# Kernel tuning notes

Measured on AMD Instinct MI355X. Metric: run time of the kernel, lower is better.

Reference implementation:

```python
import jax, jax.numpy as jnp
import numpy as np

H = 16  # num_heads (inner_dim 1024 // default head_dim 64)
D = 64  # head_dim
EPS = 1e-5

def layernorm(x, w, b):
    mu = jnp.mean(x, axis=-1, keepdims=True)
    var = jnp.var(x, axis=-1, keepdims=True)
    return (x - mu) * jax.lax.rsqrt(var + EPS) * w + b

def attention(x, kv, wq, wk, wv, wo, bo):
    b, t, c = x.shape
    s = kv.shape[1]
    q = (x @ wq).reshape(b, t, H, D).transpose(0, 2, 1, 3)   # bhtd
    k = (kv @ wk).reshape(b, s, H, D).transpose(0, 2, 1, 3)  # bhsd
    v = (kv @ wv).reshape(b, s, H, D).transpose(0, 2, 1, 3)
    scores = jnp.einsum('bhqd,bhkd->bhqk', q, k) * (D ** -0.5)
    attn = jax.nn.softmax(scores, axis=-1)
    out = jnp.einsum('bhqk,bhkd->bhqd', attn, v)
    out = out.transpose(0, 2, 1, 3).reshape(b, t, c)
    return out @ wo + bo

def setup_inputs() -> dict:
    key = jax.random.key(0)
    ks = jax.random.split(key, 16)
    hs = 1024
    dff = 4 * hs  # 4096
    sc = lambda fan_in: 1.0 / np.sqrt(fan_in)
    inp = {
        'x': jax.random.normal(ks[0], (2, 2048, hs), jnp.float32),
        'encoder_hidden_states': jax.random.normal(ks[1], (2, 512, 64), jnp.float32),
        'ln1_w': jnp.ones((hs,), jnp.float32), 'ln1_b': jnp.zeros((hs,), jnp.float32),
        'a1_wq': jax.random.normal(ks[2], (hs, hs), jnp.float32) * sc(hs),
        'a1_wk': jax.random.normal(ks[3], (hs, hs), jnp.float32) * sc(hs),
        'a1_wv': jax.random.normal(ks[4], (hs, hs), jnp.float32) * sc(hs),
        'a1_wo': jax.random.normal(ks[5], (hs, hs), jnp.float32) * sc(hs),
        'a1_bo': jnp.zeros((hs,), jnp.float32),
        'ln2_w': jnp.ones((hs,), jnp.float32), 'ln2_b': jnp.zeros((hs,), jnp.float32),
        'a2_wq': jax.random.normal(ks[6], (hs, hs), jnp.float32) * sc(hs),
        'a2_wk': jax.random.normal(ks[7], (64, hs), jnp.float32) * sc(64),
        'a2_wv': jax.random.normal(ks[8], (64, hs), jnp.float32) * sc(64),
        'a2_wo': jax.random.normal(ks[9], (hs, hs), jnp.float32) * sc(hs),
        'a2_bo': jnp.zeros((hs,), jnp.float32),
        'ln3_w': jnp.ones((hs,), jnp.float32), 'ln3_b': jnp.zeros((hs,), jnp.float32),
        'ff_w1': jax.random.normal(ks[10], (hs, 2 * dff), jnp.float32) * sc(hs),
        'ff_b1': jnp.zeros((2 * dff,), jnp.float32),
        'ff_w2': jax.random.normal(ks[11], (dff, hs), jnp.float32) * sc(dff),
        'ff_b2': jnp.zeros((hs,), jnp.float32),
    }
    return inp

def reference(x, encoder_hidden_states, ln1_w, ln1_b, a1_wq, a1_wk, a1_wv, a1_wo, a1_bo,
              ln2_w, ln2_b, a2_wq, a2_wk, a2_wv, a2_wo, a2_bo,
              ln3_w, ln3_b, ff_w1, ff_b1, ff_w2, ff_b2):
    # self-attention sub-block
    h = layernorm(x, ln1_w, ln1_b)
    x = x + attention(h, h, a1_wq, a1_wk, a1_wv, a1_wo, a1_bo)
    # cross-attention sub-block (kv from encoder_hidden_states, dim 64)
    h = layernorm(x, ln2_w, ln2_b)
    x = x + attention(h, encoder_hidden_states, a2_wq, a2_wk, a2_wv, a2_wo, a2_bo)
    # GEGLU feed-forward sub-block
    h = layernorm(x, ln3_w, ln3_b)
    hp = h @ ff_w1 + ff_b1
    h1, h2 = jnp.split(hp, 2, axis=-1)
    h = (h1 * jax.nn.gelu(h2, approximate=False)) @ ff_w2 + ff_b2
    return x + h
```

## Files before the change

kernel.cpp:

```cpp
#include <hip/hip_runtime.h>
#include <hip/hip_bf16.h>
#include <stdint.h>

typedef unsigned short u16;
typedef __bf16 bf16x8 __attribute__((ext_vector_type(8)));
typedef float f32x4 __attribute__((ext_vector_type(4)));
typedef u16 u16x8 __attribute__((ext_vector_type(8)));
typedef u16 u16x4 __attribute__((ext_vector_type(4)));

__device__ __forceinline__ u16 f2bf(float f) {
  union { float f; uint32_t u; } v; v.f = f;
  uint32_t r = v.u + 0x7fffu + ((v.u >> 16) & 1u);
  return (u16)(r >> 16);
}
__device__ __forceinline__ float bf2f(u16 u) {
  union { uint32_t u; float f; } v; v.u = ((uint32_t)u) << 16;
  return v.f;
}
__device__ __forceinline__ uint32_t cvtpk(float a, float b) {
  uint32_t r;
  asm("v_cvt_pk_bf16_f32 %0, %1, %2" : "=v"(r) : "v"(a), "v"(b));
  return r;
}

__device__ __forceinline__ void gld16(const u16* g, u16* l) {
  __builtin_amdgcn_global_load_lds(
      (const __attribute__((address_space(1))) uint32_t*)g,
      (__attribute__((address_space(3))) uint32_t*)l, 16, 0, 0);
}

struct WB {
  const float* src[6];
  u16* dst[6];
  float scale[6];
};
__global__ void wconv_b(WB wb, int K, int N) {
  const int z = blockIdx.z;
  const float* __restrict__ W = wb.src[z];
  u16* __restrict__ Wt = wb.dst[z];
  const float scale = wb.scale[z];
  __shared__ float tile[32][33];
  const int n0 = blockIdx.x * 32, k0 = blockIdx.y * 32;
  const int tx = threadIdx.x, ty = threadIdx.y;
#pragma unroll
  for (int i = 0; i < 4; ++i)
    tile[ty + 8 * i][tx] = W[(size_t)(k0 + ty + 8 * i) * N + n0 + tx];
  __syncthreads();
#pragma unroll
  for (int i = 0; i < 4; ++i)
    Wt[(size_t)(n0 + ty + 8 * i) * K + k0 + tx] = f2bf(scale * tile[tx][ty + 8 * i]);
}

__global__ void wconv_t(const float* __restrict__ W, u16* __restrict__ Wt, int K, int N) {
  __shared__ float tile[32][33];
  const int n0 = blockIdx.x * 32, k0 = blockIdx.y * 32;
  const int tx = threadIdx.x, ty = threadIdx.y;
#pragma unroll
  for (int i = 0; i < 4; ++i)
    tile[ty + 8 * i][tx] = W[(size_t)(k0 + ty + 8 * i) * N + n0 + tx];
  __syncthreads();
#pragma unroll
  for (int i = 0; i < 4; ++i)
    Wt[(size_t)(n0 + ty + 8 * i) * K + k0 + tx] = f2bf(tile[tx][ty + 8 * i]);
}

__global__ void wconv_g(const float* __restrict__ W, u16* __restrict__ Wt) {
  __shared__ float tile[32][33];
  const int n0 = blockIdx.x * 32, k0 = blockIdx.y * 32;
  const int tx = threadIdx.x, ty = threadIdx.y;
#pragma unroll
  for (int i = 0; i < 4; ++i)
    tile[ty + 8 * i][tx] = W[(size_t)(k0 + ty + 8 * i) * 8192 + n0 + tx];
  __syncthreads();
#pragma unroll
  for (int i = 0; i < 4; ++i) {
    const int n = n0 + ty + 8 * i;
    const int half = n >> 12, c = n & 4095;
    const int blk = c >> 7, cc = c & 127;
    const int wcol = cc >> 5, rem = cc & 31;
    const int sub = rem >> 4, idx = rem & 15;
    const int p = blk * 256 + wcol * 64 + (sub * 2 + half) * 16 + idx;
    Wt[(size_t)p * 1024 + k0 + tx] = f2bf(tile[tx][ty + 8 * i]);
  }
}

__global__ void cvt_bf(const float* __restrict__ in, u16* __restrict__ out, int n) {
  int i = blockIdx.x * 256 + threadIdx.x;
  if (i < n) out[i] = f2bf(in[i]);
}

__global__ __launch_bounds__(256)
void vtrans(const u16* __restrict__ V, int ldv, int hoff, u16* __restrict__ Vt, int S) {
  __shared__ u16 tile[64][72];
  const int t0 = blockIdx.x, bh = blockIdx.y;
  const int b = bh >> 4, hc = (bh & 15) * 64 + hoff;
  const int tid = threadIdx.x;
  const int r = tid >> 2, dq = (tid & 3) * 16;
  const int pos = ((r >> 5) << 5) | (((r >> 2) & 3) << 3) | (((r >> 4) & 1) << 2) | (r & 3);
  const size_t grow = ((size_t)b * S + t0 * 64 + r) * ldv + hc + dq;
  u16x8 v1 = *(const u16x8*)&V[grow];
  u16x8 v2 = *(const u16x8*)&V[grow + 8];
#pragma unroll
  for (int j = 0; j < 8; ++j) {
    tile[dq + j][pos] = v1[j];
    tile[dq + 8 + j][pos] = v2[j];
  }
  __syncthreads();
  const int d = tid >> 2, c = (tid & 3) * 16;
  u16x8 o1, o2;
#pragma unroll
  for (int j = 0; j < 8; ++j) { o1[j] = tile[d][c + j]; o2[j] = tile[d][c + 8 + j]; }
  *(u16x8*)&Vt[((size_t)bh * 64 + d) * S + t0 * 64 + c] = o1;
  *(u16x8*)&Vt[((size_t)bh * 64 + d) * S + t0 * 64 + c + 8] = o2;
}

__global__ __launch_bounds__(256)
void ln_fwd(const float* __restrict__ X, const float* __restrict__ wt,
            const float* __restrict__ bs, u16* __restrict__ Y) {
  const int row = blockIdx.x, t = threadIdx.x;
  const float4 v = *(const float4*)&X[(size_t)row * 1024 + t * 4];
  float s = v.x + v.y + v.z + v.w;
  float s2 = v.x * v.x + v.y * v.y + v.z * v.z + v.w * v.w;
#pragma unroll
  for (int off = 32; off > 0; off >>= 1) {
    s += __shfl_xor(s, off);
    s2 += __shfl_xor(s2, off);
  }
  __shared__ float rs[4], rs2[4];
  const int w = t >> 6;
  if ((t & 63) == 0) { rs[w] = s; rs2[w] = s2; }
  __syncthreads();
  s = rs[0] + rs[1] + rs[2] + rs[3];
  s2 = rs2[0] + rs2[1] + rs2[2] + rs2[3];
  const float mu = s * (1.0f / 1024.0f);
  const float var = s2 * (1.0f / 1024.0f) - mu * mu;
  const float rstd = rsqrtf(var + 1e-5f);
  const float4 wv = *(const float4*)&wt[t * 4];
  const float4 bv = *(const float4*)&bs[t * 4];
  u16x4 o;
  o[0] = f2bf((v.x - mu) * rstd * wv.x + bv.x);
  o[1] = f2bf((v.y - mu) * rstd * wv.y + bv.y);
  o[2] = f2bf((v.z - mu) * rstd * wv.z + bv.z);
  o[3] = f2bf((v.w - mu) * rstd * wv.w + bv.w);
  *(u16x4*)&Y[(size_t)row * 1024 + t * 4] = o;
}

#define GSTAGE(kt, bufi)                                                         \
  {                                                                              \
    _Pragma("unroll")                                                            \
    for (int p = 0; p < 4; ++p) {                                                \
      int idx = p * 256 + tid;                                                   \
      int row = idx >> 3, c = idx & 7;                                           \
      gld16(A + (size_t)(bm + row) * lda + (kt) * 64 + ((c ^ (row & 7)) << 3),   \
            &Al[bufi][idx * 8]);                                                 \
    }                                                                            \
    _Pragma("unroll")                                                            \
    for (int p = 0; p < TN / 32; ++p) {                                          \
      int idx = p * 256 + tid;                                                   \
      int row = idx >> 3, c = idx & 7;                                           \
      gld16(Bt + (size_t)(bn + row) * K + (kt) * 64 + ((c ^ (row & 7)) << 3),    \
            &Bl[bufi][idx * 8]);                                                 \
    }                                                                            \
  }

template<int TN>
__global__ __launch_bounds__(256, 3)
void gemm_bf16(const u16* __restrict__ A, int lda, const u16* __restrict__ Bt,
               int M, int N, int K, const float* __restrict__ bias,
               const float* __restrict__ resid, float oscale,
               float* __restrict__ outF, u16* __restrict__ outB) {
  constexpr int WNV = (TN == 128) ? 2 : 1;
  constexpr int WMV = 4 / WNV;
  constexpr int WM = 128 / WMV;
  constexpr int WN = TN / WNV;
  constexpr int MI = WM / 16, NI = WN / 16;
  __shared__ __align__(16) u16 Al[2][128 * 64];
  __shared__ __align__(16) u16 Bl[2][TN * 64];
  const int tid = threadIdx.x;
  const int w = tid >> 6, l = tid & 63, lo = l & 15, g = l >> 4;
  const int gx = gridDim.x, nwg = gx * gridDim.y;
  const int lin = blockIdx.y * gx + blockIdx.x;
  const int q = nwg >> 3, r = nwg & 7;
  const int xcd = lin & 7, pos = lin >> 3;
  const int sid = (xcd < r ? xcd * (q + 1) : r * (q + 1) + (xcd - r) * q) + pos;
  const int bm = (sid % gx) * 128, bn = (sid / gx) * TN;
  const int wm = (w / WNV) * WM, wn = (w % WNV) * WN;
  const int swz = (lo & 7) << 3;
  const int NT = K >> 6;
  f32x4 acc[MI][NI] = {};

  GSTAGE(0, 0);
  asm volatile("s_waitcnt vmcnt(0)" ::: "memory");
  __syncthreads();

  for (int t = 0; t < NT; ++t) {
    const int cur = t & 1;
    if (t + 1 < NT) GSTAGE(t + 1, cur ^ 1);
#pragma unroll
    for (int ks = 0; ks < 2; ++ks) {
      bf16x8 af[MI], bf[NI];
#pragma unroll
      for (int i = 0; i < MI; ++i)
        af[i] = *(const bf16x8*)&Al[cur][(wm + i * 16 + lo) * 64 + ((ks * 32 + g * 8) ^ swz)];
#pragma unroll
      for (int i = 0; i < NI; ++i)
        bf[i] = *(const bf16x8*)&Bl[cur][(wn + i * 16 + lo) * 64 + ((ks * 32 + g * 8) ^ swz)];
#pragma unroll
      for (int mi = 0; mi < MI; ++mi)
#pragma unroll
        for (int ni = 0; ni < NI; ++ni)
          acc[mi][ni] = __builtin_amdgcn_mfma_f32_16x16x32_bf16(af[mi], bf[ni], acc[mi][ni], 0, 0, 0);
    }
    asm volatile("s_waitcnt vmcnt(0)" ::: "memory");
    __syncthreads();
  }

#pragma unroll
  for (int mi = 0; mi < MI; ++mi) {
#pragma unroll
    for (int ni = 0; ni < NI; ++ni) {
      const int col = bn + wn + ni * 16 + lo;
      const float bb = bias ? bias[col] : 0.0f;
      const int row0 = bm + wm + mi * 16 + g * 4;
#pragma unroll
      for (int rr = 0; rr < 4; ++rr) {
        const size_t off = (size_t)(row0 + rr) * N + col;
        float v = acc[mi][ni][rr] * oscale + bb;
        if (resid) v += resid[off];
        if (outF) outF[off] = v;
        else outB[off] = f2bf(v);
      }
    }
  }
}

#define ST2(p0, p1, dst) { gld16(p0, (dst) + tid * 8); gld16(p1, (dst) + 4096 + tid * 8); (p0) += 64; (p1) += 64; }

template<int MODE>
__global__ __launch_bounds__(512, 2)
void gemm256(const u16* __restrict__ A, int lda, const u16* __restrict__ Bt,
             int M, int N, int K, const float* __restrict__ bias,
             const float* __restrict__ resid, float oscale,
             float* __restrict__ outF, u16* __restrict__ outB) {
  __shared__ __align__(16) u16 sm[65536];
  const int tid = threadIdx.x;
  const int w = tid >> 6, l = tid & 63, lo = l & 15, g = l >> 4;
  const int wrow = w >> 2, wcol = w & 3;
  const int gx = gridDim.x;
  const int nwg = gx * gridDim.y;
  const int lin = blockIdx.y * gx + blockIdx.x;
  const int q = nwg >> 3, r = nwg & 7;
  const int xcd = lin & 7, pos = lin >> 3;
  const int sid = (xcd < r ? xcd * (q + 1) : r * (q + 1) + (xcd - r) * q) + pos;
  const int bm = (sid % gx) * 256, bn = (sid / gx) * 256;

  const int NT = K >> 6;
  const int swz = (lo & 7) << 3;
  f32x4 acc[8][4] = {};

  const int sr8 = tid >> 3;
  const int sc8 = ((tid & 7) ^ (sr8 & 7)) << 3;
  const u16 *pA0 = A + (size_t)(bm + sr8) * lda + sc8;
  const u16 *pA1 = A + (size_t)(bm + 64 + sr8) * lda + sc8;
  const u16 *pA2 = A + (size_t)(bm + 128 + sr8) * lda + sc8;
  const u16 *pA3 = A + (size_t)(bm + 192 + sr8) * lda + sc8;
  const u16 *pB0 = Bt + (size_t)(bn + sr8) * K + sc8;
  const u16 *pB1 = Bt + (size_t)(bn + 64 + sr8) * K + sc8;
  const u16 *pB2 = Bt + (size_t)(bn + 128 + sr8) * K + sc8;
  const u16 *pB3 = Bt + (size_t)(bn + 192 + sr8) * K + sc8;

  ST2(pB0, pB1, sm + 16384);
  ST2(pB2, pB3, sm + 16384 + 8192);
  ST2(pA0, pA1, sm);
  ST2(pA2, pA3, sm + 8192);
  if (NT > 1) {
    ST2(pB0, pB1, sm + 32768 + 16384);
    ST2(pB2, pB3, sm + 32768 + 16384 + 8192);
    ST2(pA0, pA1, sm + 32768);
  }
  asm volatile("s_waitcnt vmcnt(6)" ::: "memory");
  __builtin_amdgcn_s_barrier();

  for (int t = 0; t < NT; ++t) {
    u16* Ab_ = sm + (t & 1) * 32768;
    u16* Bb_ = Ab_ + 16384;
    bf16x8 a0[4][2], a1[4][2], bfr[4][2];
#pragma unroll
    for (int mf = 0; mf < 4; ++mf) {
      const int rowi = wrow * 128 + mf * 16 + lo;
#pragma unroll
      for (int kk = 0; kk < 2; ++kk)
        a0[mf][kk] = *(const bf16x8*)&Ab_[rowi * 64 + ((kk * 32 + g * 8) ^ swz)];
    }
#pragma unroll
    for (int nf = 0; nf < 4; ++nf) {
      const int rowi = wcol * 64 + nf * 16 + lo;
#pragma unroll
      for (int kk = 0; kk < 2; ++kk)
        bfr[nf][kk] = *(const bf16x8*)&Bb_[rowi * 64 + ((kk * 32 + g * 8) ^ swz)];
    }
    if (t + 1 < NT)
      ST2(pA2, pA3, sm + ((t + 1) & 1) * 32768 + 8192);
    __builtin_amdgcn_s_barrier();
    __builtin_amdgcn_s_setprio(1);
#pragma unroll
    for (int mf = 0; mf < 4; ++mf)
#pragma unroll
      for (int nf = 0; nf < 2; ++nf)
#pragma unroll
        for (int kk = 0; kk < 2; ++kk)
          acc[mf][nf] = __builtin_amdgcn_mfma_f32_16x16x32_bf16(a0[mf][kk], bfr[nf][kk], acc[mf][nf], 0, 0, 0);
    __builtin_amdgcn_s_setprio(0);
    __builtin_amdgcn_s_barrier();
#pragma unroll
    for (int mf = 0; mf < 4; ++mf) {
      const int rowi = wrow * 128 + 64 + mf * 16 + lo;
#pragma unroll
      for (int kk = 0; kk < 2; ++kk)
        a1[mf][kk] = *(const bf16x8*)&Ab_[rowi * 64 + ((kk * 32 + g * 8) ^ swz)];
    }
    if (t + 2 < NT)
      ST2(pB0, pB1, sm + (t & 1) * 32768 + 16384);
    __builtin_amdgcn_s_barrier();
    __builtin_amdgcn_s_setprio(1);
#pragma unroll
    for (int mf = 0; mf < 4; ++mf)
#pragma unroll
      for (int nf = 2; nf < 4; ++nf)
#pragma unroll
        for (int kk = 0; kk < 2; ++kk)
          acc[mf][nf] = __builtin_amdgcn_mfma_f32_16x16x32_bf16(a0[mf][kk], bfr[nf][kk], acc[mf][nf], 0, 0, 0);
    __builtin_amdgcn_s_setprio(0);
    __builtin_amdgcn_s_barrier();
    if (t + 2 < NT)
      ST2(pB2, pB3, sm + (t & 1) * 32768 + 16384 + 8192);
    __builtin_amdgcn_s_barrier();
    __builtin_amdgcn_s_setprio(1);
#pragma unroll
    for (int mf = 0; mf < 4; ++mf)
#pragma unroll
      for (int nf = 0; nf < 2; ++nf)
#pragma unroll
        for (int kk = 0; kk < 2; ++kk)
          acc[4 + mf][nf] = __builtin_amdgcn_mfma_f32_16x16x32_bf16(a1[mf][kk], bfr[nf][kk], acc[4 + mf][nf], 0, 0, 0);
    __builtin_amdgcn_s_setprio(0);
    __builtin_amdgcn_s_barrier();
    if (t + 2 < NT)
      ST2(pA0, pA1, sm + (t & 1) * 32768);
    __builtin_amdgcn_s_barrier();
    __builtin_amdgcn_s_setprio(1);
#pragma unroll
    for (int mf = 0; mf < 4; ++mf)
#pragma unroll
      for (int nf = 2; nf < 4; ++nf)
#pragma unroll
        for (int kk = 0; kk < 2; ++kk)
          acc[4 + mf][nf] = __builtin_amdgcn_mfma_f32_16x16x32_bf16(a1[mf][kk], bfr[nf][kk], acc[4 + mf][nf], 0, 0, 0);
    __builtin_amdgcn_s_setprio(0);
    if (t + 2 < NT) asm volatile("s_waitcnt vmcnt(6)" ::: "memory");
    else            asm volatile("s_waitcnt vmcnt(0)" ::: "memory");
    __builtin_amdgcn_s_barrier();
  }

  if (MODE == 1) {
    const int obase = bn >> 1;
#pragma unroll
    for (int mi = 0; mi < 8; ++mi) {
#pragma unroll
      for (int sub = 0; sub < 2; ++sub) {
        const int col = obase + wcol * 32 + sub * 16 + lo;
        const float b1 = bias[col];
        const float b2 = bias[4096 + col];
#pragma unroll
        for (int rr = 0; rr < 4; ++rr) {
          const int rowi = wrow * 128 + mi * 16 + g * 4 + rr;
          const float h1 = acc[mi][sub * 2][rr] + b1;
          const float h2 = acc[mi][sub * 2 + 1][rr] + b2;
          const float ge = 0.5f * h2 * (1.0f + erff(h2 * 0.70710678118f));
          outB[(size_t)(bm + rowi) * 4096 + col] = f2bf(h1 * ge);
        }
      }
    }
    return;
  }

#pragma unroll
  for (int mi = 0; mi < 8; ++mi) {
#pragma unroll
    for (int ni = 0; ni < 4; ++ni) {
      const int col = bn + wcol * 64 + ni * 16 + lo;
      const float bb = bias ? bias[col] : 0.0f;
      const int row0 = bm + wrow * 128 + mi * 16 + g * 4;
#pragma unroll
      for (int rr = 0; rr < 4; ++rr) {
        const size_t off = (size_t)(row0 + rr) * N + col;
        float v = acc[mi][ni][rr] * oscale + bb;
        if (resid) v += resid[off];
        if (outF) outF[off] = v;
        else outB[off] = f2bf(v);
      }
    }
  }
}

#define ABODY(TT, KST, KRD, VST, VRD, SCur, SNxt)                                  \
  {                                                                                \
    if ((TT) + 2 < ntile) {                                                        \
      gld16(kp0, &KST[tid * 8]);                                                   \
      gld16(kp1, &KST[2048 + tid * 8]);                                            \
      kp0 += kadv; kp1 += kadv;                                                    \
    }                                                                              \
    if ((TT) + 1 < ntile) {                                                        \
      gld16(vp0, &VST[tid * 8]);                                                   \
      gld16(vp1, &VST[2048 + tid * 8]);                                            \
      vp0 += 64; vp1 += 64;                                                        \
    }                                                                              \
    if ((TT) + 2 < ntile)      asm volatile("s_waitcnt vmcnt(4)" ::: "memory");    \
    else if ((TT) + 1 < ntile) asm volatile("s_waitcnt vmcnt(2)" ::: "memory");    \
    else                       asm volatile("s_waitcnt vmcnt(0)" ::: "memory");    \
    __builtin_amdgcn_s_barrier();                                                  \
    if ((TT) + 1 < ntile) {                                                        \
      _Pragma("unroll")                                                            \
      for (int c = 0; c < 4; ++c) {                                                \
        f32x4 zz = {};                                                             \
        SNxt[c] = zz;                                                              \
        _Pragma("unroll")                                                          \
        for (int kk = 0; kk < 2; ++kk) {                                           \
          bf16x8 kf = *(const bf16x8*)&KRD[(c * 16 + lo) * 64 +                    \
                                           ((kk * 32 + g * 8) ^ ((lo & 7) << 3))]; \
          SNxt[c] = __builtin_amdgcn_mfma_f32_16x16x32_bf16(kf, qf[kk], SNxt[c], 0, 0, 0); \
        }                                                                          \
      }                                                                            \
    }                                                                              \
    float mx = fmaxf(fmaxf(fmaxf(SCur[0][0], SCur[0][1]), fmaxf(SCur[0][2], SCur[0][3])),  \
                     fmaxf(fmaxf(SCur[1][0], SCur[1][1]), fmaxf(SCur[1][2], SCur[1][3]))); \
    mx = fmaxf(mx, fmaxf(fmaxf(fmaxf(SCur[2][0], SCur[2][1]), fmaxf(SCur[2][2], SCur[2][3])),  \
                         fmaxf(fmaxf(SCur[3][0], SCur[3][1]), fmaxf(SCur[3][2], SCur[3][3])))); \
    mx = fmaxf(mx, __shfl_xor(mx, 16));                                            \
    mx = fmaxf(mx, __shfl_xor(mx, 32));                                            \
    if (!__all(mx <= m + 8.0f)) {                                                  \
      const float mn = fmaxf(m, mx);                                               \
      const float al = exp2f(m - mn);                                              \
      m = mn;                                                                      \
      f32x4 arv;                                                                   \
      _Pragma("unroll")                                                            \
      for (int rr = 0; rr < 4; ++rr) arv[rr] = __shfl(al, 20 * g + rr);            \
      _Pragma("unroll")                                                            \
      for (int dn = 0; dn < 4; ++dn) oa[dn] *= arv;                                \
      lrow *= arv;                                                                 \
    }                                                                              \
    _Pragma("unroll")                                                              \
    for (int c = 0; c < 4; ++c)                                                    \
      _Pragma("unroll")                                                            \
      for (int rr = 0; rr < 4; ++rr)                                               \
        SCur[c][rr] = exp2f(SCur[c][rr] - m);                                      \
    union { uint32_t u[4]; bf16x8 v; } af[2];                                      \
    _Pragma("unroll")                                                              \
    for (int ks = 0; ks < 2; ++ks) {                                               \
      af[ks].u[0] = cvtpk(SCur[2 * ks][0], SCur[2 * ks][1]);                       \
      af[ks].u[1] = cvtpk(SCur[2 * ks][2], SCur[2 * ks][3]);                       \
      af[ks].u[2] = cvtpk(SCur[2 * ks + 1][0], SCur[2 * ks + 1][1]);               \
      af[ks].u[3] = cvtpk(SCur[2 * ks + 1][2], SCur[2 * ks + 1][3]);               \
    }                                                                              \
    lrow = __builtin_amdgcn_mfma_f32_16x16x32_bf16(af[0].v, onesc.v, lrow, 0, 0, 0); \
    lrow = __builtin_amdgcn_mfma_f32_16x16x32_bf16(af[1].v, onesc.v, lrow, 0, 0, 0); \
    _Pragma("unroll")                                                              \
    for (int dn = 0; dn < 4; ++dn)                                                 \
      _Pragma("unroll")                                                            \
      for (int ks = 0; ks < 2; ++ks) {                                             \
        bf16x8 vf = *(const bf16x8*)&VRD[(dn * 16 + lo) * 64 +                     \
                                         ((ks * 32 + g * 8) ^ ((lo & 7) << 3))];   \
        oa[dn] = __builtin_amdgcn_mfma_f32_16x16x32_bf16(af[ks].v, vf, oa[dn], 0, 0, 0); \
      }                                                                            \
    asm volatile("s_waitcnt lgkmcnt(0)" ::: "memory");                             \
    __builtin_amdgcn_s_barrier();                                                  \
  }

__global__ __launch_bounds__(256, 4)
void attn_fwd(const u16* __restrict__ Q, int ldq, const u16* __restrict__ K, int ldk,
              const u16* __restrict__ Vt, u16* __restrict__ O, int T, int S) {
  __shared__ __align__(16) u16 Kl[2][4096];
  __shared__ __align__(16) u16 Vl[2][4096];
  const int tid = threadIdx.x, w = tid >> 6, l = tid & 63, lo = l & 15, g = l >> 4;
  const int nwg = gridDim.x * gridDim.y;
  const int n = blockIdx.y * gridDim.x + blockIdx.x;
  const int sid = (n & 7) * (nwg >> 3) + (n >> 3);
  const int qt = sid % gridDim.x, bh = sid / gridDim.x;
  const int b = bh >> 4, h = bh & 15, hc = h * 64;
  const int q0 = qt * 64 + w * 16;
  const size_t qrow = (size_t)b * T + q0;
  const size_t krow0 = (size_t)b * S;
  const size_t vrow0 = (size_t)bh * 64;

  bf16x8 qf[2];
#pragma unroll
  for (int kk = 0; kk < 2; ++kk)
    qf[kk] = *(const bf16x8*)&Q[(qrow + lo) * ldq + hc + kk * 32 + g * 8];

  union { u16 u[8]; bf16x8 v; } onesc;
#pragma unroll
  for (int j = 0; j < 8; ++j) onesc.u[j] = 0x3F80;

  f32x4 oa[4] = {};
  f32x4 lrow = {};
  float m = -1e30f;

  const int srow = tid >> 3;
  const int scol = (((tid & 7) ^ (srow & 7)) << 3);
  const int ntile = S >> 6;
  const size_t kadv = (size_t)64 * ldk;

  const u16* kp0 = K + (krow0 + 128 + srow) * ldk + hc + scol;
  const u16* kp1 = K + (krow0 + 160 + srow) * ldk + hc + scol;
  const u16* vp0 = Vt + (vrow0 + srow) * S + 64 + scol;
  const u16* vp1 = Vt + (vrow0 + 32 + srow) * S + 64 + scol;

#pragma unroll
  for (int c = 0; c < 2; ++c)
    gld16(K + (krow0 + c * 32 + srow) * ldk + hc + scol, &Kl[0][c * 2048 + tid * 8]);
#pragma unroll
  for (int c = 0; c < 2; ++c)
    gld16(K + (krow0 + 64 + c * 32 + srow) * ldk + hc + scol, &Kl[1][c * 2048 + tid * 8]);
#pragma unroll
  for (int c = 0; c < 2; ++c)
    gld16(Vt + (vrow0 + c * 32 + srow) * S + scol, &Vl[0][c * 2048 + tid * 8]);
  asm volatile("s_waitcnt vmcnt(0)" ::: "memory");
  __builtin_amdgcn_s_barrier();

  f32x4 sC[4] = {}, sN[4] = {};
#pragma unroll
  for (int c = 0; c < 4; ++c)
#pragma unroll
    for (int kk = 0; kk < 2; ++kk) {
      bf16x8 kf = *(const bf16x8*)&Kl[0][(c * 16 + lo) * 64 +
                                        ((kk * 32 + g * 8) ^ ((lo & 7) << 3))];
      sC[c] = __builtin_amdgcn_mfma_f32_16x16x32_bf16(kf, qf[kk], sC[c], 0, 0, 0);
    }
  asm volatile("s_waitcnt lgkmcnt(0)" ::: "memory");
  __builtin_amdgcn_s_barrier();

  for (int t0 = 0; t0 < ntile; t0 += 2) {
    ABODY(t0,     Kl[0], Kl[1], Vl[1], Vl[0], sC, sN)
    ABODY(t0 + 1, Kl[1], Kl[0], Vl[0], Vl[1], sN, sC)
  }

#pragma unroll
  for (int dn = 0; dn < 4; ++dn)
#pragma unroll
    for (int rr = 0; rr < 4; ++rr)
      O[(qrow + g * 4 + rr) * 1024 + hc + dn * 16 + lo] = f2bf(oa[dn][rr] / lrow[rr]);
}

extern "C" void kernel_launch(void* const* d_in, const int* in_sizes, int n_in,
                              void* d_out, int out_size, void* d_ws, size_t ws_size,
                              hipStream_t stream) {
  const float* x      = (const float*)d_in[0];
  const float* enc    = (const float*)d_in[1];
  const float* ln1_w  = (const float*)d_in[2];
  const float* ln1_b  = (const float*)d_in[3];
  const float* a1_wq  = (const float*)d_in[4];
  const float* a1_wk  = (const float*)d_in[5];
  const float* a1_wv  = (const float*)d_in[6];
  const float* a1_wo  = (const float*)d_in[7];
  const float* a1_bo  = (const float*)d_in[8];
  const float* ln2_w  = (const float*)d_in[9];
  const float* ln2_b  = (const float*)d_in[10];
  const float* a2_wq  = (const float*)d_in[11];
  const float* a2_wk  = (const float*)d_in[12];
  const float* a2_wv  = (const float*)d_in[13];
  const float* a2_wo  = (const float*)d_in[14];
  const float* a2_bo  = (const float*)d_in[15];
  const float* ln3_w  = (const float*)d_in[16];
  const float* ln3_b  = (const float*)d_in[17];
  const float* ff_w1  = (const float*)d_in[18];
  const float* ff_b1  = (const float*)d_in[19];
  const float* ff_w2  = (const float*)d_in[20];
  const float* ff_b2  = (const float*)d_in[21];

  char* ws = (char*)d_ws;
  const size_t MB = 1u << 20;
  u16* wqkv1t = (u16*)(ws + 0 * MB);
  u16* wo1t   = (u16*)(ws + 6 * MB);
  u16* wq2t   = (u16*)(ws + 8 * MB);
  u16* wo2t   = (u16*)(ws + 10 * MB);
  u16* wkv2t  = (u16*)(ws + 12 * MB);
  u16* encb   = (u16*)(ws + 12 * MB + 512 * 1024);
  u16* w1t    = (u16*)(ws + 13 * MB);
  u16* w2t    = (u16*)(ws + 29 * MB);
  float* x2   = (float*)(ws + 37 * MB);
  u16* Vt1    = (u16*)(ws + 37 * MB);
  u16* Vt2    = (u16*)(ws + 45 * MB);
  u16* KVb    = (u16*)(ws + 47 * MB);
  u16* hbuf   = (u16*)(ws + 53 * MB);
  u16* qkv    = (u16*)(ws + 61 * MB);
  u16* Qb     = (u16*)(ws + 61 * MB);
  u16* Ab     = (u16*)(ws + 85 * MB);
  float* x1   = (float*)(ws + 93 * MB);
  u16* gq     = (u16*)(ws + 61 * MB);

  const float SCL = 0.125f * 1.44269504f;
  const dim3 tb(32, 8);
  {
    WB wb;
    wb.src[0] = a1_wq; wb.dst[0] = wqkv1t;               wb.scale[0] = SCL;
    wb.src[1] = a1_wk; wb.dst[1] = wqkv1t + 1024 * 1024; wb.scale[1] = 1.0f;
    wb.src[2] = a1_wv; wb.dst[2] = wqkv1t + 2048 * 1024; wb.scale[2] = 1.0f;
    wb.src[3] = a1_wo; wb.dst[3] = wo1t;                 wb.scale[3] = 1.0f;
    wb.src[4] = a2_wq; wb.dst[4] = wq2t;                 wb.scale[4] = SCL;
    wb.src[5] = a2_wo; wb.dst[5] = wo2t;                 wb.scale[5] = 1.0f;
    wconv_b<<<dim3(32, 32, 6), tb, 0, stream>>>(wb, 1024, 1024);
    WB wb2;
    wb2.src[0] = a2_wk; wb2.dst[0] = wkv2t;             wb2.scale[0] = 1.0f;
    wb2.src[1] = a2_wv; wb2.dst[1] = wkv2t + 64 * 1024; wb2.scale[1] = 1.0f;
    wb2.src[2] = a2_wk; wb2.dst[2] = wkv2t;             wb2.scale[2] = 1.0f;
    wb2.src[3] = a2_wk; wb2.dst[3] = wkv2t;             wb2.scale[3] = 1.0f;
    wb2.src[4] = a2_wk; wb2.dst[4] = wkv2t;             wb2.scale[4] = 1.0f;
    wb2.src[5] = a2_wk; wb2.dst[5] = wkv2t;             wb2.scale[5] = 1.0f;
    wconv_b<<<dim3(32, 2, 2), tb, 0, stream>>>(wb2, 64, 1024);
  }
  wconv_g<<<dim3(256, 32), tb, 0, stream>>>(ff_w1, w1t);
  wconv_t<<<dim3(32, 128), tb, 0, stream>>>(ff_w2, w2t, 4096, 1024);
  cvt_bf<<<256, 256, 0, stream>>>(enc, encb, 2 * 512 * 64);

  ln_fwd<<<4096, 256, 0, stream>>>(x, ln1_w, ln1_b, hbuf);
  gemm256<0><<<dim3(16, 12), 512, 0, stream>>>(hbuf, 1024, wqkv1t, 4096, 3072, 1024, nullptr, nullptr, 1.0f, nullptr, qkv);
  vtrans<<<dim3(32, 32), 256, 0, stream>>>(qkv, 3072, 2048, Vt1, 2048);
  attn_fwd<<<dim3(32, 32), 256, 0, stream>>>(qkv, 3072, qkv + 1024, 3072, Vt1, Ab, 2048, 2048);
  gemm_bf16<64><<<dim3(32, 16), 256, 0, stream>>>(Ab, 1024, wo1t, 4096, 1024, 1024, a1_bo, x, 1.0f, x1, nullptr);

  ln_fwd<<<4096, 256, 0, stream>>>(x1, ln2_w, ln2_b, hbuf);
  gemm_bf16<64><<<dim3(32, 16), 256, 0, stream>>>(hbuf, 1024, wq2t, 4096, 1024, 1024, nullptr, nullptr, 1.0f, nullptr, Qb);
  gemm_bf16<64><<<dim3(8, 32), 256, 0, stream>>>(encb, 64, wkv2t, 1024, 2048, 64, nullptr, nullptr, 1.0f, nullptr, KVb);
  vtrans<<<dim3(8, 32), 256, 0, stream>>>(KVb + 1024, 2048, 0, Vt2, 512);
  attn_fwd<<<dim3(32, 32), 256, 0, stream>>>(Qb, 1024, KVb, 2048, Vt2, Ab, 2048, 512);
  gemm_bf16<64><<<dim3(32, 16), 256, 0, stream>>>(Ab, 1024, wo2t, 4096, 1024, 1024, a2_bo, x1, 1.0f, x2, nullptr);

  ln_fwd<<<4096, 256, 0, stream>>>(x2, ln3_w, ln3_b, hbuf);
  gemm256<1><<<dim3(16, 32), 512, 0, stream>>>(hbuf, 1024, w1t, 4096, 8192, 1024, ff_b1, nullptr, 1.0f, nullptr, gq);
  gemm_bf16<64><<<dim3(32, 16), 256, 0, stream>>>(gq, 4096, w2t, 4096, 1024, 4096, ff_b2, x2, 1.0f, (float*)d_out, nullptr);
}
```

Measured before the change: 397.9 us.

## Enlarge attention query tile to 256 rows with two 16-row blocks per wave

The attention kernel now uses 512-thread workgroups covering 256 query rows, and each wave handles two 16-row query blocks that share every K and V fragment read from LDS. Each thread issues one K and one V global-to-LDS load per tile instead of two. This cuts LDS read traffic and K/V global loads per query row by reusing fragments across more MFMAs. In exchange the grid has 4x fewer workgroups, and register pressure rises from doubled accumulators, which may lower occupancy.

New measurement: 405.9 us. +2.0%, slower.

```diff
diff --git a/kernel.cpp b/kernel.cpp
--- a/kernel.cpp
+++ b/kernel.cpp
@@ -403,152 +403,156 @@
   }
 }
 
-#define ABODY(TT, KST, KRD, VST, VRD, SCur, SNxt)                                  \
+#define ABODY2(TT, KST, KRD, VST, VRD, SCur, SNxt)                                 \
   {                                                                                \
-    if ((TT) + 2 < ntile) {                                                        \
-      gld16(kp0, &KST[tid * 8]);                                                   \
-      gld16(kp1, &KST[2048 + tid * 8]);                                            \
-      kp0 += kadv; kp1 += kadv;                                                    \
-    }                                                                              \
-    if ((TT) + 1 < ntile) {                                                        \
-      gld16(vp0, &VST[tid * 8]);                                                   \
-      gld16(vp1, &VST[2048 + tid * 8]);                                            \
-      vp0 += 64; vp1 += 64;                                                        \
-    }                                                                              \
-    if ((TT) + 2 < ntile)      asm volatile("s_waitcnt vmcnt(4)" ::: "memory");    \
-    else if ((TT) + 1 < ntile) asm volatile("s_waitcnt vmcnt(2)" ::: "memory");    \
+    if ((TT) + 2 < ntile) { gld16(kp, &KST[tid * 8]); kp += kadv; }                \
+    if ((TT) + 1 < ntile) { gld16(vp, &VST[tid * 8]); vp += 64; }                  \
+    if ((TT) + 2 < ntile)      asm volatile("s_waitcnt vmcnt(2)" ::: "memory");    \
+    else if ((TT) + 1 < ntile) asm volatile("s_waitcnt vmcnt(1)" ::: "memory");    \
     else                       asm volatile("s_waitcnt vmcnt(0)" ::: "memory");    \
     __builtin_amdgcn_s_barrier();                                                  \
     if ((TT) + 1 < ntile) {                                                        \
       _Pragma("unroll")                                                            \
-      for (int c = 0; c < 4; ++c) {                                                \
-        f32x4 zz = {};                                                             \
-        SNxt[c] = zz;                                                              \
+      for (int j = 0; j < 2; ++j)                                                  \
+        _Pragma("unroll")                                                          \
+        for (int c = 0; c < 4; ++c) { f32x4 zz = {}; SNxt[j][c] = zz; }            \
+      _Pragma("unroll")                                                            \
+      for (int c = 0; c < 4; ++c)                                                  \
         _Pragma("unroll")                                                          \
         for (int kk = 0; kk < 2; ++kk) {                                           \
           bf16x8 kf = *(const bf16x8*)&KRD[(c * 16 + lo) * 64 +                    \
-                                           ((kk * 32 + g * 8) ^ ((lo & 7) << 3))]; \
-          SNxt[c] = __builtin_amdgcn_mfma_f32_16x16x32_bf16(kf, qf[kk], SNxt[c], 0, 0, 0); \
+                                           ((kk * 32 + g * 8) ^ swz8)];            \
+          SNxt[0][c] = __builtin_amdgcn_mfma_f32_16x16x32_bf16(kf, qf[0][kk], SNxt[0][c], 0, 0, 0); \
+          SNxt[1][c] = __builtin_amdgcn_mfma_f32_16x16x32_bf16(kf, qf[1][kk], SNxt[1][c], 0, 0, 0); \
         }                                                                          \
+    }                                                                              \
+    float mxj[2];                                                                  \
+    _Pragma("unroll")                                                              \
+    for (int j = 0; j < 2; ++j) {                                                  \
+      float mx = fmaxf(fmaxf(fmaxf(SCur[j][0][0], SCur[j][0][1]), fmaxf(SCur[j][0][2], SCur[j][0][3])),  \
+                       fmaxf(fmaxf(SCur[j][1][0], SCur[j][1][1]), fmaxf(SCur[j][1][2], SCur[j][1][3]))); \
+      mx = fmaxf(mx, fmaxf(fmaxf(fmaxf(SCur[j][2][0], SCur[j][2][1]), fmaxf(SCur[j][2][2], SCur[j][2][3])),  \
+                           fmaxf(fmaxf(SCur[j][3][0], SCur[j][3][1]), fmaxf(SCur[j][3][2], SCur[j][3][3])))); \
+      mx = fmaxf(mx, __shfl_xor(mx, 16));                                          \
+      mx = fmaxf(mx, __shfl_xor(mx, 32));                                          \
+      mxj[j] = mx;                                                                 \
+    }                                                                              \
+    if (!__all(mxj[0] <= mreg[0] + 8.0f && mxj[1] <= mreg[1] + 8.0f)) {            \
+      _Pragma("unroll")                                                            \
+      for (int j = 0; j < 2; ++j) {                                                \
+        const float mn = fmaxf(mreg[j], mxj[j]);                                   \
+        const float al = exp2f(mreg[j] - mn);                                      \
+        mreg[j] = mn;                                                              \
+        f32x4 arv;                                                                 \
+        _Pragma("unroll")                                                          \
+        for (int rr = 0; rr < 4; ++rr) arv[rr] = __shfl(al, 20 * g + rr);          \
+        _Pragma("unroll")                                                          \
+        for (int dn = 0; dn < 4; ++dn) oa[j][dn] *= arv;                           \
+        lrow2[j] *= arv;                                                           \
       }                                                                            \
     }                                                                              \
-    float mx = fmaxf(fmaxf(fmaxf(SCur[0][0], SCur[0][1]), fmaxf(SCur[0][2], SCur[0][3])),  \
-                     fmaxf(fmaxf(SCur[1][0], SCur[1][1]), fmaxf(SCur[1][2], SCur[1][3]))); \
-    mx = fmaxf(mx, fmaxf(fmaxf(fmaxf(SCur[2][0], SCur[2][1]), fmaxf(SCur[2][2], SCur[2][3])),  \
-                         fmaxf(fmaxf(SCur[3][0], SCur[3][1]), fmaxf(SCur[3][2], SCur[3][3])))); \
-    mx = fmaxf(mx, __shfl_xor(mx, 16));                                            \
-    mx = fmaxf(mx, __shfl_xor(mx, 32));                                            \
-    if (!__all(mx <= m + 8.0f)) {                                                  \
-      const float mn = fmaxf(m, mx);                                               \
-      const float al = exp2f(m - mn);                                              \
-      m = mn;                                                                      \
-      f32x4 arv;                                                                   \
+    union { uint32_t u[4]; bf16x8 v; } af[2][2];                                   \
+    _Pragma("unroll")                                                              \
+    for (int j = 0; j < 2; ++j) {                                                  \
       _Pragma("unroll")                                                            \
-      for (int rr = 0; rr < 4; ++rr) arv[rr] = __shfl(al, 20 * g + rr);            \
+      for (int c = 0; c < 4; ++c)                                                  \
+        _Pragma("unroll")                                                          \
+        for (int rr = 0; rr < 4; ++rr)                                             \
+          SCur[j][c][rr] = exp2f(SCur[j][c][rr] - mreg[j]);                        \
       _Pragma("unroll")                                                            \
-      for (int dn = 0; dn < 4; ++dn) oa[dn] *= arv;                                \
-      lrow *= arv;                                                                 \
+      for (int ks = 0; ks < 2; ++ks) {                                             \
+        af[j][ks].u[0] = cvtpk(SCur[j][2 * ks][0], SCur[j][2 * ks][1]);            \
+        af[j][ks].u[1] = cvtpk(SCur[j][2 * ks][2], SCur[j][2 * ks][3]);            \
+        af[j][ks].u[2] = cvtpk(SCur[j][2 * ks + 1][0], SCur[j][2 * ks + 1][1]);    \
+        af[j][ks].u[3] = cvtpk(SCur[j][2 * ks + 1][2], SCur[j][2 * ks + 1][3]);    \
+      }                                                                            \
+      lrow2[j] = __builtin_amdgcn_mfma_f32_16x16x32_bf16(af[j][0].v, onesc.v, lrow2[j], 0, 0, 0); \
+      lrow2[j] = __builtin_amdgcn_mfma_f32_16x16x32_bf16(af[j][1].v, onesc.v, lrow2[j], 0, 0, 0); \
     }                                                                              \
-    _Pragma("unroll")                                                              \
-    for (int c = 0; c < 4; ++c)                                                    \
-      _Pragma("unroll")                                                            \
-      for (int rr = 0; rr < 4; ++rr)                                               \
-        SCur[c][rr] = exp2f(SCur[c][rr] - m);                                      \
-    union { uint32_t u[4]; bf16x8 v; } af[2];                                      \
-    _Pragma("unroll")                                                              \
-    for (int ks = 0; ks < 2; ++ks) {                                               \
-      af[ks].u[0] = cvtpk(SCur[2 * ks][0], SCur[2 * ks][1]);                       \
-      af[ks].u[1] = cvtpk(SCur[2 * ks][2], SCur[2 * ks][3]);                       \
-      af[ks].u[2] = cvtpk(SCur[2 * ks + 1][0], SCur[2 * ks + 1][1]);               \
-      af[ks].u[3] = cvtpk(SCur[2 * ks + 1][2], SCur[2 * ks + 1][3]);               \
-    }                                                                              \
-    lrow = __builtin_amdgcn_mfma_f32_16x16x32_bf16(af[0].v, onesc.v, lrow, 0, 0, 0); \
-    lrow = __builtin_amdgcn_mfma_f32_16x16x32_bf16(af[1].v, onesc.v, lrow, 0, 0, 0); \
     _Pragma("unroll")                                                              \
     for (int dn = 0; dn < 4; ++dn)                                                 \
       _Pragma("unroll")                                                            \
       for (int ks = 0; ks < 2; ++ks) {                                             \
         bf16x8 vf = *(const bf16x8*)&VRD[(dn * 16 + lo) * 64 +                     \
-                                         ((ks * 32 + g * 8) ^ ((lo & 7) << 3))];   \
-        oa[dn] = __builtin_amdgcn_mfma_f32_16x16x32_bf16(af[ks].v, vf, oa[dn], 0, 0, 0); \
+                                         ((ks * 32 + g * 8) ^ swz8)];              \
+        oa[0][dn] = __builtin_amdgcn_mfma_f32_16x16x32_bf16(af[0][ks].v, vf, oa[0][dn], 0, 0, 0); \
+        oa[1][dn] = __builtin_amdgcn_mfma_f32_16x16x32_bf16(af[1][ks].v, vf, oa[1][dn], 0, 0, 0); \
       }                                                                            \
     asm volatile("s_waitcnt lgkmcnt(0)" ::: "memory");                             \
     __builtin_amdgcn_s_barrier();                                                  \
   }
 
-__global__ __launch_bounds__(256, 4)
+__global__ __launch_bounds__(512, 2)
 void attn_fwd(const u16* __restrict__ Q, int ldq, const u16* __restrict__ K, int ldk,
               const u16* __restrict__ Vt, u16* __restrict__ O, int T, int S) {
   __shared__ __align__(16) u16 Kl[2][4096];
   __shared__ __align__(16) u16 Vl[2][4096];
   const int tid = threadIdx.x, w = tid >> 6, l = tid & 63, lo = l & 15, g = l >> 4;
+  const int swz8 = (lo & 7) << 3;
   const int nwg = gridDim.x * gridDim.y;
   const int n = blockIdx.y * gridDim.x + blockIdx.x;
   const int sid = (n & 7) * (nwg >> 3) + (n >> 3);
   const int qt = sid % gridDim.x, bh = sid / gridDim.x;
   const int b = bh >> 4, h = bh & 15, hc = h * 64;
-  const int q0 = qt * 64 + w * 16;
+  const int q0 = qt * 256 + w * 32;
   const size_t qrow = (size_t)b * T + q0;
   const size_t krow0 = (size_t)b * S;
   const size_t vrow0 = (size_t)bh * 64;
 
-  bf16x8 qf[2];
-#pragma unroll
-  for (int kk = 0; kk < 2; ++kk)
-    qf[kk] = *(const bf16x8*)&Q[(qrow + lo) * ldq + hc + kk * 32 + g * 8];
+  bf16x8 qf[2][2];
+#pragma unroll
+  for (int j = 0; j < 2; ++j)
+#pragma unroll
+    for (int kk = 0; kk < 2; ++kk)
+      qf[j][kk] = *(const bf16x8*)&Q[(qrow + j * 16 + lo) * ldq + hc + kk * 32 + g * 8];
 
   union { u16 u[8]; bf16x8 v; } onesc;
 #pragma unroll
   for (int j = 0; j < 8; ++j) onesc.u[j] = 0x3F80;
 
-  f32x4 oa[4] = {};
-  f32x4 lrow = {};
-  float m = -1e30f;
-
-  const int srow = tid >> 3;
-  const int scol = (((tid & 7) ^ (srow & 7)) << 3);
+  f32x4 oa[2][4] = {};
+  f32x4 lrow2[2] = {};
+  float mreg[2] = {-1e30f, -1e30f};
+
+  const int sr = tid >> 3;
+  const int scol = (((tid & 7) ^ (sr & 7)) << 3);
   const int ntile = S >> 6;
   const size_t kadv = (size_t)64 * ldk;
 
-  const u16* kp0 = K + (krow0 + 128 + srow) * ldk + hc + scol;
-  const u16* kp1 = K + (krow0 + 160 + srow) * ldk + hc + scol;
-  const u16* vp0 = Vt + (vrow0 + srow) * S + 64 + scol;
-  const u16* vp1 = Vt + (vrow0 + 32 + srow) * S + 64 + scol;
-
-#pragma unroll
-  for (int c = 0; c < 2; ++c)
-    gld16(K + (krow0 + c * 32 + srow) * ldk + hc + scol, &Kl[0][c * 2048 + tid * 8]);
-#pragma unroll
-  for (int c = 0; c < 2; ++c)
-    gld16(K + (krow0 + 64 + c * 32 + srow) * ldk + hc + scol, &Kl[1][c * 2048 + tid * 8]);
-#pragma unroll
-  for (int c = 0; c < 2; ++c)
-    gld16(Vt + (vrow0 + c * 32 + srow) * S + scol, &Vl[0][c * 2048 + tid * 8]);
+  const u16* kp = K + (krow0 + 128 + sr) * ldk + hc + scol;
+  const u16* vp = Vt + (vrow0 + sr) * S + 64 + scol;
+
+  gld16(K + (krow0 + sr) * ldk + hc + scol, &Kl[0][tid * 8]);
+  gld16(K + (krow0 + 64 + sr) * ldk + hc + scol, &Kl[1][tid * 8]);
+  gld16(Vt + (vrow0 + sr) * S + scol, &Vl[0][tid * 8]);
   asm volatile("s_waitcnt vmcnt(0)" ::: "memory");
   __builtin_amdgcn_s_barrier();
 
-  f32x4 sC[4] = {}, sN[4] = {};
+  f32x4 sC[2][4] = {}, sN[2][4] = {};
 #pragma unroll
   for (int c = 0; c < 4; ++c)
 #pragma unroll
     for (int kk = 0; kk < 2; ++kk) {
-      bf16x8 kf = *(const bf16x8*)&Kl[0][(c * 16 + lo) * 64 +
-                                        ((kk * 32 + g * 8) ^ ((lo & 7) << 3))];
-      sC[c] = __builtin_amdgcn_mfma_f32_16x16x32_bf16(kf, qf[kk], sC[c], 0, 0, 0);
+      bf16x8 kf = *(const bf16x8*)&Kl[0][(c * 16 + lo) * 64 + ((kk * 32 + g * 8) ^ swz8)];
+      sC[0][c] = __builtin_amdgcn_mfma_f32_16x16x32_bf16(kf, qf[0][kk], sC[0][c], 0, 0, 0);
+      sC[1][c] = __builtin_amdgcn_mfma_f32_16x16x32_bf16(kf, qf[1][kk], sC[1][c], 0, 0, 0);
     }
   asm volatile("s_waitcnt lgkmcnt(0)" ::: "memory");
   __builtin_amdgcn_s_barrier();
 
   for (int t0 = 0; t0 < ntile; t0 += 2) {
-    ABODY(t0,     Kl[0], Kl[1], Vl[1], Vl[0], sC, sN)
-    ABODY(t0 + 1, Kl[1], Kl[0], Vl[0], Vl[1], sN, sC)
-  }
-
-#pragma unroll
-  for (int dn = 0; dn < 4; ++dn)
-#pragma unroll
-    for (int rr = 0; rr < 4; ++rr)
-      O[(qrow + g * 4 + rr) * 1024 + hc + dn * 16 + lo] = f2bf(oa[dn][rr] / lrow[rr]);
+    ABODY2(t0,     Kl[0], Kl[1], Vl[1], Vl[0], sC, sN)
+    ABODY2(t0 + 1, Kl[1], Kl[0], Vl[0], Vl[1], sN, sC)
+  }
+
+#pragma unroll
+  for (int j = 0; j < 2; ++j)
+#pragma unroll
+    for (int dn = 0; dn < 4; ++dn)
+#pragma unroll
+      for (int rr = 0; rr < 4; ++rr)
+        O[(qrow + j * 16 + g * 4 + rr) * 1024 + hc + dn * 16 + lo] =
+            f2bf(oa[j][dn][rr] / lrow2[j][rr]);
 }
 
 extern "C" void kernel_launch(void* const* d_in, const int* in_sizes, int n_in,
@@ -625,14 +629,14 @@
   ln_fwd<<<4096, 256, 0, stream>>>(x, ln1_w, ln1_b, hbuf);
   gemm256<0><<<dim3(16, 12), 512, 0, stream>>>(hbuf, 1024, wqkv1t, 4096, 3072, 1024, nullptr, nullptr, 1.0f, nullptr, qkv);
   vtrans<<<dim3(32, 32), 256, 0, stream>>>(qkv, 3072, 2048, Vt1, 2048);
-  attn_fwd<<<dim3(32, 32), 256, 0, stream>>>(qkv, 3072, qkv + 1024, 3072, Vt1, Ab, 2048, 2048);
+  attn_fwd<<<dim3(8, 32), 512, 0, stream>>>(qkv, 3072, qkv + 1024, 3072, Vt1, Ab, 2048, 2048);
   gemm_bf16<64><<<dim3(32, 16), 256, 0, stream>>>(Ab, 1024, wo1t, 4096, 1024, 1024, a1_bo, x, 1.0f, x1, nullptr);
 
   ln_fwd<<<4096, 256, 0, stream>>>(x1, ln2_w, ln2_b, hbuf);
   gemm_bf16<64><<<dim3(32, 16), 256, 0, stream>>>(hbuf, 1024, wq2t, 4096, 1024, 1024, nullptr, nullptr, 1.0f, nullptr, Qb);
   gemm_bf16<64><<<dim3(8, 32), 256, 0, stream>>>(encb, 64, wkv2t, 1024, 2048, 64, nullptr, nullptr, 1.0f, nullptr, KVb);
   vtrans<<<dim3(8, 32), 256, 0, stream>>>(KVb + 1024, 2048, 0, Vt2, 512);
-  attn_fwd<<<dim3(32, 32), 256, 0, stream>>>(Qb, 1024, KVb, 2048, Vt2, Ab, 2048, 512);
+  attn_fwd<<<dim3(8, 32), 512, 0, stream>>>(Qb, 1024, KVb, 2048, Vt2, Ab, 2048, 512);
   gemm_bf16<64><<<dim3(32, 16), 256, 0, stream>>>(Ab, 1024, wo2t, 4096, 1024, 1024, a2_bo, x1, 1.0f, x2, nullptr);
 
   ln_fwd<<<4096, 256, 0, stream>>>(x2, ln3_w, ln3_b, hbuf);
```
